# Performance work log

Measured on AMD Instinct MI355X. Metric: run time of the kernel, lower is better.

Reference implementation:

```python
import jax, jax.numpy as jnp
import numpy as np

N, D, H = 4096, 1024, 8
DH = D // H
EPS = 1e-5


def layer_norm(x, g, b):
    mu = jnp.mean(x, axis=-1, keepdims=True)
    var = jnp.mean(jnp.square(x - mu), axis=-1, keepdims=True)
    return (x - mu) * jax.lax.rsqrt(var + EPS) * g + b


def setup_inputs() -> dict:
    key = jax.random.key(0)
    ks = jax.random.split(key, 12)
    s = 0.02
    inp = {
        "x": jax.random.normal(ks[0], (N, D), dtype=jnp.float32),
        "adj": (jax.random.uniform(ks[1], (N, N)) < 0.01).astype(jnp.float32),
        "Wq": jax.random.normal(ks[2], (D, D), dtype=jnp.float32) * s,
        "Wk": jax.random.normal(ks[3], (D, D), dtype=jnp.float32) * s,
        "Wv": jax.random.normal(ks[4], (D, D), dtype=jnp.float32) * s,
        "Wo_w": jax.random.normal(ks[5], (D, D), dtype=jnp.float32) * s,
        "Wo_b": jnp.zeros((D,), dtype=jnp.float32),
        "adj_bias": jnp.full((H,), 1.0, dtype=jnp.float32),
        "ln1_g": jnp.ones((D,), dtype=jnp.float32),
        "ln1_b": jnp.zeros((D,), dtype=jnp.float32),
        "ffn_ln_g": jnp.ones((D,), dtype=jnp.float32),
        "ffn_ln_b": jnp.zeros((D,), dtype=jnp.float32),
        "ffn_w1": jax.random.normal(ks[6], (D, 2 * D), dtype=jnp.float32) * s,
        "ffn_b1": jnp.zeros((2 * D,), dtype=jnp.float32),
        "ffn_w2": jax.random.normal(ks[7], (2 * D, D), dtype=jnp.float32) * s,
        "ffn_b2": jnp.zeros((D,), dtype=jnp.float32),
    }
    return inp


def reference(x, adj, Wq, Wk, Wv, Wo_w, Wo_b, adj_bias, ln1_g, ln1_b,
              ffn_ln_g, ffn_ln_b, ffn_w1, ffn_b1, ffn_w2, ffn_b2):
    scale = DH ** -0.5
    Q = (x @ Wq).reshape(N, H, DH)
    K = (x @ Wk).reshape(N, H, DH)
    V = (x @ Wv).reshape(N, H, DH)
    # attn[i,h,j] = <Q_i, K_j> * scale + beta_h * adj[i,j]
    attn = jnp.einsum('bhd,nhd->bhn', Q, K) * scale
    attn = attn + adj_bias[None, :, None] * adj[:, None, :]
    attn = jax.nn.softmax(attn, axis=-1)  # dropout in eval mode -> identity
    out = jnp.einsum('bhn,nhd->bhd', attn, V).reshape(N, D)
    out = out @ Wo_w + Wo_b
    h = layer_norm(x + out, ln1_g, ln1_b)
    f = layer_norm(h, ffn_ln_g, ffn_ln_b)
    f = jax.nn.gelu(f @ ffn_w1 + ffn_b1, approximate=False) @ ffn_w2 + ffn_b2
    return h + f
```

## Files before the change

kernel.cpp:

```cpp
#include <hip/hip_runtime.h>
#include <hip/hip_bf16.h>
#include <cstdint>
#include <cstddef>

typedef __hip_bfloat16 bf16;
typedef __attribute__((ext_vector_type(8))) short short8;
typedef __attribute__((ext_vector_type(4))) short short4v;
typedef __attribute__((ext_vector_type(4))) float floatx4;
typedef unsigned long long u64;

#define DEVI static __device__ __forceinline__

DEVI void load_lds16(const void* g, void* l) {
  __builtin_amdgcn_global_load_lds((const __attribute__((address_space(1))) unsigned int*)g,
                                   (__attribute__((address_space(3))) unsigned int*)l, 16, 0, 0);
}
DEVI short8 ld8(const bf16* p) { return *(const short8*)p; }
DEVI floatx4 mfma16(short8 a, short8 b, floatx4 c) {
  return __builtin_amdgcn_mfma_f32_16x16x32_bf16(a, b, c, 0, 0, 0);
}
DEVI floatx4 mfma1k(short4v a, short4v b, floatx4 c) {
  return __builtin_amdgcn_mfma_f32_16x16x16bf16_1k(a, b, c, 0, 0, 0);
}
DEVI short bfb(float f) { bf16 h = __float2bfloat16(f); return __builtin_bit_cast(short, h); }
DEVI float fbf(short s) { bf16 h = __builtin_bit_cast(bf16, s); return __bfloat162float(h); }

DEVI void tr_tile(const float* in, bf16* out, int R, int C, int bx, int by) {
  __shared__ float t[32][33];
  int c0 = bx * 32, r0 = by * 32;
  int tx = threadIdx.x & 31, ty = threadIdx.x >> 5;
#pragma unroll
  for (int i = 0; i < 32; i += 8) t[ty + i][tx] = in[(size_t)(r0 + ty + i) * C + c0 + tx];
  __syncthreads();
#pragma unroll
  for (int i = 0; i < 32; i += 8)
    out[(size_t)(c0 + ty + i) * R + r0 + tx] = __float2bfloat16(t[tx][ty + i]);
}

__global__ __launch_bounds__(256)
void prep_all(const float* __restrict__ x, bf16* __restrict__ xb,
              const float* __restrict__ adj, u64* __restrict__ bits,
              const float* Wq, const float* Wk, const float* Wv, const float* Wo,
              const float* W1, const float* W2,
              bf16* Wqkvt, bf16* Wot, bf16* W1t, bf16* W2t) {
  int id = blockIdx.x;
  if (id < 4096) {
    const int row = id, tid = threadIdx.x;
    const int wave = tid >> 6, lane = tid & 63;
    float4 v = ((const float4*)(x + (size_t)row * 1024))[tid];
    bf16* o = xb + (size_t)row * 1024 + tid * 4;
    o[0] = __float2bfloat16(v.x); o[1] = __float2bfloat16(v.y);
    o[2] = __float2bfloat16(v.z); o[3] = __float2bfloat16(v.w);
    const float* arow = adj + (size_t)row * 4096;
#pragma unroll
    for (int it = 0; it < 16; it++) {
      int col = it * 256 + tid;
      u64 m = __ballot(arow[col] != 0.f);
      if (lane == 0) bits[(size_t)row * 64 + it * 4 + wave] = m;
    }
  } else if (id < 8192) {
    int q = id - 4096, w = q >> 10, t = q & 1023;
    const float* in = w == 0 ? Wq : w == 1 ? Wk : w == 2 ? Wv : Wo;
    bf16* out = w == 0 ? Wqkvt : w == 1 ? Wqkvt + 1024ull * 1024
              : w == 2 ? Wqkvt + 2048ull * 1024 : Wot;
    tr_tile(in, out, 1024, 1024, t & 31, t >> 5);
  } else if (id < 10240) {
    int t = id - 8192;
    tr_tile(W1, W1t, 1024, 2048, t & 63, t >> 6);
  } else {
    int t = id - 10240;
    tr_tile(W2, W2t, 2048, 1024, t & 31, t >> 5);
  }
}

__global__ __launch_bounds__(256)
void tr_bf16t(const bf16* __restrict__ in, bf16* __restrict__ out, int inLd) {
  __shared__ bf16 t[32][33];
  int c0 = blockIdx.x * 32, r0 = blockIdx.y * 32;
  int tx = threadIdx.x, ty = threadIdx.y;
#pragma unroll
  for (int i = 0; i < 32; i += 8) t[ty + i][tx] = in[(size_t)(r0 + ty + i) * inLd + c0 + tx];
  __syncthreads();
#pragma unroll
  for (int i = 0; i < 32; i += 8)
    out[(size_t)(c0 + ty + i) * 4096 + r0 + tx] = t[tx][ty + i];
}

template <int MODE>
__global__ __launch_bounds__(256)
void gemm_bt(const bf16* __restrict__ A, const bf16* __restrict__ Bt,
             const float* __restrict__ bias, const float* __restrict__ resid,
             float* __restrict__ outF, bf16* __restrict__ outB,
             int M, int Nn, int K) {
  __shared__ alignas(16) bf16 As[3][128 * 32];
  __shared__ alignas(16) bf16 Bs[3][128 * 32];
  const int tid = threadIdx.x;
  const int wave = tid >> 6, lane = tid & 63;
  const int m0 = blockIdx.y * 128, n0 = blockIdx.x * 128;
  const int wr = (wave >> 1) * 64, wc = (wave & 1) * 64;
  const int l15 = lane & 15, qq = lane >> 4;
  const int lr = lane >> 2, l4 = lane & 3;
  const int Kspan = K / gridDim.z;
  const int kbeg = blockIdx.z * Kspan;
  const int T = Kspan >> 5;

  floatx4 acc[4][4];
#pragma unroll
  for (int i = 0; i < 4; i++)
#pragma unroll
    for (int j = 0; j < 4; j++) acc[i][j] = (floatx4)0.f;

  const bf16* gA0 = A + (size_t)(m0 + wave * 16 + lr) * K + kbeg + l4 * 8;
  const bf16* gA1 = gA0 + (size_t)64 * K;
  const bf16* gB0 = Bt + (size_t)(n0 + wave * 16 + lr) * K + kbeg + l4 * 8;
  const bf16* gB1 = gB0 + (size_t)64 * K;
  const int lo = wave * 16 * 32;

  auto stage = [&](int t, int buf) {
    int kt = t * 32;
    load_lds16(gA0 + kt, &As[buf][lo]);
    load_lds16(gA1 + kt, &As[buf][64 * 32 + lo]);
    load_lds16(gB0 + kt, &Bs[buf][lo]);
    load_lds16(gB1 + kt, &Bs[buf][64 * 32 + lo]);
  };
  stage(0, 0);
  stage(1, 1);

  int bc = 0;
  for (int t = 0; t < T; ++t) {
    if (t < T - 1) asm volatile("s_waitcnt vmcnt(4) lgkmcnt(0)" ::: "memory");
    else           asm volatile("s_waitcnt vmcnt(0) lgkmcnt(0)" ::: "memory");
    __builtin_amdgcn_s_barrier();
    if (t + 2 < T) { int bs = bc == 0 ? 2 : bc - 1; stage(t + 2, bs); }

    short8 af[4], bfr[4];
#pragma unroll
    for (int mi = 0; mi < 4; mi++) af[mi] = ld8(&As[bc][(wr + mi * 16 + l15) * 32 + qq * 8]);
#pragma unroll
    for (int ni = 0; ni < 4; ni++) bfr[ni] = ld8(&Bs[bc][(wc + ni * 16 + l15) * 32 + qq * 8]);
#pragma unroll
    for (int mi = 0; mi < 4; mi++)
#pragma unroll
      for (int ni = 0; ni < 4; ni++)
        acc[mi][ni] = mfma16(af[mi], bfr[ni], acc[mi][ni]);
    bc = bc == 2 ? 0 : bc + 1;
  }

  const size_t zoff = (size_t)blockIdx.z * M * Nn;
#pragma unroll
  for (int mi = 0; mi < 4; mi++) {
    int row = m0 + wr + mi * 16 + qq * 4;
#pragma unroll
    for (int ni = 0; ni < 4; ni++) {
      int col = n0 + wc + ni * 16 + l15;
      float bv = 0.f;
      if (MODE == 2) bv = bias[col];
      if (MODE == 4 && blockIdx.z == 0) bv = bias[col];
#pragma unroll
      for (int r = 0; r < 4; r++) {
        float v = acc[mi][ni][r] + bv;
        size_t off = (size_t)(row + r) * Nn + col;
        if (MODE == 0) {
          outB[off] = __float2bfloat16(v);
        } else if (MODE == 2) {
          outB[off] = __float2bfloat16(0.5f * v * (1.f + erff(v * 0.70710678118654752f)));
        } else {
          if (resid && blockIdx.z == 1) v += resid[off];
          outF[zoff + off] = v;
        }
      }
    }
  }
}

__global__ __launch_bounds__(256, 2)
void attn_kernel(const bf16* __restrict__ QKV, const bf16* __restrict__ Vt,
                 const u64* __restrict__ adjbits, const float* __restrict__ adj_bias,
                 bf16* __restrict__ AOpart, float* __restrict__ lpart) {
  __shared__ alignas(16) bf16 Kf[16 * 512];
  __shared__ alignas(16) bf16 Vf[16 * 512];
  const int q0 = blockIdx.x * 128;
  const int h = blockIdx.y;
  const int split = blockIdx.z;
  const int k0 = split * 1024;
  const int tid = threadIdx.x, wave = tid >> 6, lane = tid & 63;
  const int l15 = lane & 15, qq = lane >> 4;
  const float beta = adj_bias[h];
  const float scale = 0.08838834764831845f;

  short8 qf[2][4];
#pragma unroll
  for (int mi = 0; mi < 2; mi++)
#pragma unroll
    for (int kk = 0; kk < 4; kk++)
      qf[mi][kk] = ld8(&QKV[(size_t)(q0 + wave * 32 + mi * 16 + l15) * 3072 +
                            h * 128 + kk * 32 + qq * 8]);

  floatx4 o[2][8];
#pragma unroll
  for (int mi = 0; mi < 2; mi++)
#pragma unroll
    for (int d = 0; d < 8; d++) o[mi][d] = (floatx4)0.f;
  float lrow[2] = {0.f, 0.f};

  const size_t abase = (size_t)(q0 + wave * 32 + l15) * 64 + split * 16;

  for (int t = 0; t < 16; t++) {
    const int kt = k0 + t * 64;
    __syncthreads();
#pragma unroll
    for (int i = 0; i < 4; i++) {
      int fi = wave * 4 + i;
      int ni = fi >> 2, kk = fi & 3;
      load_lds16(&QKV[(size_t)(kt + ni * 16 + l15) * 3072 + 1024 + h * 128 + kk * 32 + qq * 8],
                 (char*)Kf + fi * 1024);
      int d = fi >> 1, k2 = fi & 1;
      load_lds16(&Vt[(size_t)(h * 128 + d * 16 + l15) * 4096 + kt + k2 * 32 + qq * 8],
                 (char*)Vf + fi * 1024);
    }
    u64 ab0 = adjbits[abase + t];
    u64 ab1 = adjbits[abase + 16 * 64 + t];
    asm volatile("s_waitcnt vmcnt(0)" ::: "memory");
    __syncthreads();

#pragma unroll
    for (int ni = 0; ni < 4; ni++) {
      floatx4 s0 = (floatx4)0.f, s1 = (floatx4)0.f;
#pragma unroll
      for (int kk = 0; kk < 4; kk++) {
        short8 kf = ld8(&Kf[(ni * 4 + kk) * 512 + lane * 8]);
        s0 = mfma16(kf, qf[0][kk], s0);
        s1 = mfma16(kf, qf[1][kk], s1);
      }
      short4v pa0, pa1;
      {
        float p0, p1, p2, p3;
        int bp = ni * 16 + qq * 4;
        p0 = __expf(fmaf(s0[0], scale, ((ab0 >> (bp + 0)) & 1) ? beta : 0.f));
        p1 = __expf(fmaf(s0[1], scale, ((ab0 >> (bp + 1)) & 1) ? beta : 0.f));
        p2 = __expf(fmaf(s0[2], scale, ((ab0 >> (bp + 2)) & 1) ? beta : 0.f));
        p3 = __expf(fmaf(s0[3], scale, ((ab0 >> (bp + 3)) & 1) ? beta : 0.f));
        lrow[0] += (p0 + p1) + (p2 + p3);
        pa0.x = bfb(p0); pa0.y = bfb(p1); pa0.z = bfb(p2); pa0.w = bfb(p3);
        p0 = __expf(fmaf(s1[0], scale, ((ab1 >> (bp + 0)) & 1) ? beta : 0.f));
        p1 = __expf(fmaf(s1[1], scale, ((ab1 >> (bp + 1)) & 1) ? beta : 0.f));
        p2 = __expf(fmaf(s1[2], scale, ((ab1 >> (bp + 2)) & 1) ? beta : 0.f));
        p3 = __expf(fmaf(s1[3], scale, ((ab1 >> (bp + 3)) & 1) ? beta : 0.f));
        lrow[1] += (p0 + p1) + (p2 + p3);
        pa1.x = bfb(p0); pa1.y = bfb(p1); pa1.z = bfb(p2); pa1.w = bfb(p3);
      }
      const int voff = ((ni & 1) * 2 + (qq >> 1)) * 256 + l15 * 16 + (qq & 1) * 8;
#pragma unroll
      for (int d = 0; d < 8; d++) {
        short4v vf = *(const short4v*)((const char*)Vf + (d * 2 + (ni >> 1)) * 1024 + voff);
        o[0][d] = mfma1k(pa0, vf, o[0][d]);
        o[1][d] = mfma1k(pa1, vf, o[1][d]);
      }
    }
  }

#pragma unroll
  for (int mi = 0; mi < 2; mi++) {
    float v = lrow[mi];
    v += __shfl_xor(v, 16, 64);
    v += __shfl_xor(v, 32, 64);
    if (qq == 0) lpart[((size_t)split * 4096 + q0 + wave * 32 + mi * 16 + l15) * 8 + h] = v;
#pragma unroll
    for (int r = 0; r < 4; r++) {
      int grow = q0 + wave * 32 + mi * 16 + qq * 4 + r;
      bf16* dst = AOpart + ((size_t)split * 4096 + grow) * 1024 + h * 128;
#pragma unroll
      for (int d = 0; d < 8; d++) dst[d * 16 + l15] = __float2bfloat16(o[mi][d][r]);
    }
  }
}

__global__ __launch_bounds__(256)
void attn_norm(const bf16* __restrict__ AOpart, const float* __restrict__ lpart,
               bf16* __restrict__ AO) {
  int row = blockIdx.x, tid = threadIdx.x;
  int h = tid >> 5;
  float ls = 0.f;
#pragma unroll
  for (int s = 0; s < 4; s++) ls += lpart[((size_t)s * 4096 + row) * 8 + h];
  float a0 = 0.f, a1 = 0.f, a2 = 0.f, a3 = 0.f;
#pragma unroll
  for (int s = 0; s < 4; s++) {
    short4v v = *(const short4v*)&AOpart[((size_t)s * 4096 + row) * 1024 + tid * 4];
    a0 += fbf(v.x); a1 += fbf(v.y); a2 += fbf(v.z); a3 += fbf(v.w);
  }
  float inv = 1.f / ls;
  bf16* op = AO + (size_t)row * 1024 + tid * 4;
  op[0] = __float2bfloat16(a0 * inv);
  op[1] = __float2bfloat16(a1 * inv);
  op[2] = __float2bfloat16(a2 * inv);
  op[3] = __float2bfloat16(a3 * inv);
}

DEVI void block_sum2(float& a, float& b, float* red) {
#pragma unroll
  for (int o = 1; o < 64; o <<= 1) { a += __shfl_xor(a, o, 64); b += __shfl_xor(b, o, 64); }
  int wv = threadIdx.x >> 6;
  if ((threadIdx.x & 63) == 0) { red[wv] = a; red[4 + wv] = b; }
  __syncthreads();
  a = red[0] + red[1] + red[2] + red[3];
  b = red[4] + red[5] + red[6] + red[7];
  __syncthreads();
}

__global__ __launch_bounds__(256)
void ln2_kernel(const float* __restrict__ x, const float* __restrict__ ao0,
                const float* __restrict__ ao1,
                const float* __restrict__ g1, const float* __restrict__ b1,
                const float* __restrict__ g2, const float* __restrict__ b2,
                float* __restrict__ hout, bf16* __restrict__ fln) {
  __shared__ float red[8];
  const int row = blockIdx.x, tid = threadIdx.x;
  float4 xv = ((const float4*)(x + (size_t)row * 1024))[tid];
  float4 av = ((const float4*)(ao0 + (size_t)row * 1024))[tid];
  float4 aw = ((const float4*)(ao1 + (size_t)row * 1024))[tid];
  float s0 = xv.x + av.x + aw.x, s1 = xv.y + av.y + aw.y;
  float s2 = xv.z + av.z + aw.z, s3 = xv.w + av.w + aw.w;
  float sum = s0 + s1 + s2 + s3;
  float ssq = s0 * s0 + s1 * s1 + s2 * s2 + s3 * s3;
  block_sum2(sum, ssq, red);
  float mu = sum * (1.f / 1024.f);
  float rs = rsqrtf(ssq * (1.f / 1024.f) - mu * mu + 1e-5f);
  float4 gv = ((const float4*)g1)[tid], bv = ((const float4*)b1)[tid];
  float h0 = (s0 - mu) * rs * gv.x + bv.x;
  float h1 = (s1 - mu) * rs * gv.y + bv.y;
  float h2 = (s2 - mu) * rs * gv.z + bv.z;
  float h3 = (s3 - mu) * rs * gv.w + bv.w;
  float4 hv; hv.x = h0; hv.y = h1; hv.z = h2; hv.w = h3;
  ((float4*)(hout + (size_t)row * 1024))[tid] = hv;
  float sum2 = h0 + h1 + h2 + h3;
  float ssq2 = h0 * h0 + h1 * h1 + h2 * h2 + h3 * h3;
  block_sum2(sum2, ssq2, red);
  float mu2 = sum2 * (1.f / 1024.f);
  float rs2 = rsqrtf(ssq2 * (1.f / 1024.f) - mu2 * mu2 + 1e-5f);
  float4 g2v = ((const float4*)g2)[tid], b2v = ((const float4*)b2)[tid];
  bf16* op = fln + (size_t)row * 1024 + tid * 4;
  op[0] = __float2bfloat16((h0 - mu2) * rs2 * g2v.x + b2v.x);
  op[1] = __float2bfloat16((h1 - mu2) * rs2 * g2v.y + b2v.y);
  op[2] = __float2bfloat16((h2 - mu2) * rs2 * g2v.z + b2v.z);
  op[3] = __float2bfloat16((h3 - mu2) * rs2 * g2v.w + b2v.w);
}

__global__ __launch_bounds__(256)
void add2_kernel(const float* __restrict__ a, const float* __restrict__ b,
                 float* __restrict__ o) {
  int i = blockIdx.x * 256 + threadIdx.x;
  float4 va = ((const float4*)a)[i];
  float4 vb = ((const float4*)b)[i];
  float4 vo; vo.x = va.x + vb.x; vo.y = va.y + vb.y;
  vo.z = va.z + vb.z; vo.w = va.w + vb.w;
  ((float4*)o)[i] = vo;
}

extern "C" void kernel_launch(void* const* d_in, const int* in_sizes, int n_in,
                              void* d_out, int out_size, void* d_ws, size_t ws_size,
                              hipStream_t stream) {
  const float* x    = (const float*)d_in[0];
  const float* adj  = (const float*)d_in[1];
  const float* Wq   = (const float*)d_in[2];
  const float* Wk   = (const float*)d_in[3];
  const float* Wv   = (const float*)d_in[4];
  const float* Wo   = (const float*)d_in[5];
  const float* Wob  = (const float*)d_in[6];
  const float* adjb = (const float*)d_in[7];
  const float* g1   = (const float*)d_in[8];
  const float* b1   = (const float*)d_in[9];
  const float* g2   = (const float*)d_in[10];
  const float* b2   = (const float*)d_in[11];
  const float* W1   = (const float*)d_in[12];
  const float* fb1  = (const float*)d_in[13];
  const float* W2   = (const float*)d_in[14];
  const float* fb2  = (const float*)d_in[15];
  float* out = (float*)d_out;

  char* w = (char*)d_ws;
  size_t off = 0;
  auto take = [&](size_t bytes) {
    char* p = w + off;
    off += (bytes + 255) & ~(size_t)255;
    return p;
  };
  bf16* xb    = (bf16*)take(4096ull * 1024 * 2);
  bf16* Wqkvt = (bf16*)take(3072ull * 1024 * 2);
  bf16* Wot   = (bf16*)take(1024ull * 1024 * 2);
  bf16* W1t   = (bf16*)take(2048ull * 1024 * 2);
  bf16* W2t   = (bf16*)take(1024ull * 2048 * 2);
  bf16* QKV   = (bf16*)take(4096ull * 3072 * 2);
  bf16* Vt    = (bf16*)take(1024ull * 4096 * 2);
  bf16* AO    = (bf16*)take(4096ull * 1024 * 2);
  u64*  adjbits = (u64*)take(4096ull * 64 * 8);
  float* lpart  = (float*)take(4ull * 4096 * 8 * 4);
  char* big = take(32ull << 20);
  bf16*  AOpart = (bf16*)big;
  float* WoP    = (float*)big;
  float* F2P    = (float*)big;
  float* H   = (float*)take(4096ull * 1024 * 4);
  bf16*  FLN = (bf16*)take(4096ull * 1024 * 2);
  bf16*  G   = (bf16*)take(4096ull * 2048 * 2);

  dim3 tb(32, 8);
  prep_all<<<12288, 256, 0, stream>>>(x, xb, adj, adjbits, Wq, Wk, Wv, Wo, W1, W2,
                                      Wqkvt, Wot, W1t, W2t);
  gemm_bt<0><<<dim3(24, 32, 1), 256, 0, stream>>>(xb, Wqkvt, nullptr, nullptr,
                                                  nullptr, QKV, 4096, 3072, 1024);
  tr_bf16t<<<dim3(32, 128), tb, 0, stream>>>(QKV + 2048, Vt, 3072);
  attn_kernel<<<dim3(32, 8, 4), 256, 0, stream>>>(QKV, Vt, adjbits, adjb, AOpart, lpart);
  attn_norm<<<4096, 256, 0, stream>>>(AOpart, lpart, AO);
  gemm_bt<4><<<dim3(8, 32, 2), 256, 0, stream>>>(AO, Wot, Wob, nullptr,
                                                 WoP, nullptr, 4096, 1024, 1024);
  ln2_kernel<<<4096, 256, 0, stream>>>(x, WoP, WoP + 4096ull * 1024, g1, b1, g2, b2, H, FLN);
  gemm_bt<2><<<dim3(16, 32, 1), 256, 0, stream>>>(FLN, W1t, fb1, nullptr,
                                                  nullptr, G, 4096, 2048, 1024);
  gemm_bt<4><<<dim3(8, 32, 2), 256, 0, stream>>>(G, W2t, fb2, H,
                                                 F2P, nullptr, 4096, 1024, 2048);
  add2_kernel<<<4096, 256, 0, stream>>>(F2P, F2P + 4096ull * 1024, out);
}
```

Before: 442.3 us.

## Double-buffer K/V LDS tiles and prefetch adjacency bits in attention kernel

Each K/V tile gets two LDS buffers. The next tile's global-to-LDS loads are issued before the current tile's MFMA and softmax work, and the wait is relaxed to vmcnt(8), so load latency overlaps compute instead of stalling every iteration. The adjacency bitmask words are also prefetched one iteration ahead. The cost is double the LDS per block, which may limit occupancy, and raw s_barrier calls that rely on the hand-written waitcnt ordering being correct.

```diff
diff --git a/kernel.cpp b/kernel.cpp
--- a/kernel.cpp
+++ b/kernel.cpp
@@ -177,8 +177,8 @@
 void attn_kernel(const bf16* __restrict__ QKV, const bf16* __restrict__ Vt,
                  const u64* __restrict__ adjbits, const float* __restrict__ adj_bias,
                  bf16* __restrict__ AOpart, float* __restrict__ lpart) {
-  __shared__ alignas(16) bf16 Kf[16 * 512];
-  __shared__ alignas(16) bf16 Vf[16 * 512];
+  __shared__ alignas(16) bf16 Kf[2][16 * 512];
+  __shared__ alignas(16) bf16 Vf[2][16 * 512];
   const int q0 = blockIdx.x * 128;
   const int h = blockIdx.y;
   const int split = blockIdx.z;
@@ -205,30 +205,43 @@
 
   const size_t abase = (size_t)(q0 + wave * 32 + l15) * 64 + split * 16;
 
-  for (int t = 0; t < 16; t++) {
+  auto stage = [&](int t, int buf) {
     const int kt = k0 + t * 64;
-    __syncthreads();
 #pragma unroll
     for (int i = 0; i < 4; i++) {
       int fi = wave * 4 + i;
       int ni = fi >> 2, kk = fi & 3;
       load_lds16(&QKV[(size_t)(kt + ni * 16 + l15) * 3072 + 1024 + h * 128 + kk * 32 + qq * 8],
-                 (char*)Kf + fi * 1024);
+                 (char*)Kf[buf] + fi * 1024);
       int d = fi >> 1, k2 = fi & 1;
       load_lds16(&Vt[(size_t)(h * 128 + d * 16 + l15) * 4096 + kt + k2 * 32 + qq * 8],
-                 (char*)Vf + fi * 1024);
-    }
-    u64 ab0 = adjbits[abase + t];
-    u64 ab1 = adjbits[abase + 16 * 64 + t];
-    asm volatile("s_waitcnt vmcnt(0)" ::: "memory");
-    __syncthreads();
+                 (char*)Vf[buf] + fi * 1024);
+    }
+  };
+
+  u64 a0c = adjbits[abase + 0];
+  u64 a1c = adjbits[abase + 1024 + 0];
+  stage(0, 0);
+
+  for (int t = 0; t < 16; t++) {
+    const int buf = t & 1;
+    __builtin_amdgcn_s_barrier();
+    if (t < 15) {
+      stage(t + 1, buf ^ 1);
+      asm volatile("s_waitcnt vmcnt(8)" ::: "memory");
+    } else {
+      asm volatile("s_waitcnt vmcnt(0)" ::: "memory");
+    }
+    __builtin_amdgcn_s_barrier();
+    u64 a0n = 0, a1n = 0;
+    if (t < 15) { a0n = adjbits[abase + t + 1]; a1n = adjbits[abase + 1024 + t + 1]; }
 
 #pragma unroll
     for (int ni = 0; ni < 4; ni++) {
       floatx4 s0 = (floatx4)0.f, s1 = (floatx4)0.f;
 #pragma unroll
       for (int kk = 0; kk < 4; kk++) {
-        short8 kf = ld8(&Kf[(ni * 4 + kk) * 512 + lane * 8]);
+        short8 kf = ld8(&Kf[buf][(ni * 4 + kk) * 512 + lane * 8]);
         s0 = mfma16(kf, qf[0][kk], s0);
         s1 = mfma16(kf, qf[1][kk], s1);
       }
@@ -236,27 +249,28 @@
       {
         float p0, p1, p2, p3;
         int bp = ni * 16 + qq * 4;
-        p0 = __expf(fmaf(s0[0], scale, ((ab0 >> (bp + 0)) & 1) ? beta : 0.f));
-        p1 = __expf(fmaf(s0[1], scale, ((ab0 >> (bp + 1)) & 1) ? beta : 0.f));
-        p2 = __expf(fmaf(s0[2], scale, ((ab0 >> (bp + 2)) & 1) ? beta : 0.f));
-        p3 = __expf(fmaf(s0[3], scale, ((ab0 >> (bp + 3)) & 1) ? beta : 0.f));
+        p0 = __expf(fmaf(s0[0], scale, ((a0c >> (bp + 0)) & 1) ? beta : 0.f));
+        p1 = __expf(fmaf(s0[1], scale, ((a0c >> (bp + 1)) & 1) ? beta : 0.f));
+        p2 = __expf(fmaf(s0[2], scale, ((a0c >> (bp + 2)) & 1) ? beta : 0.f));
+        p3 = __expf(fmaf(s0[3], scale, ((a0c >> (bp + 3)) & 1) ? beta : 0.f));
         lrow[0] += (p0 + p1) + (p2 + p3);
         pa0.x = bfb(p0); pa0.y = bfb(p1); pa0.z = bfb(p2); pa0.w = bfb(p3);
-        p0 = __expf(fmaf(s1[0], scale, ((ab1 >> (bp + 0)) & 1) ? beta : 0.f));
-        p1 = __expf(fmaf(s1[1], scale, ((ab1 >> (bp + 1)) & 1) ? beta : 0.f));
-        p2 = __expf(fmaf(s1[2], scale, ((ab1 >> (bp + 2)) & 1) ? beta : 0.f));
-        p3 = __expf(fmaf(s1[3], scale, ((ab1 >> (bp + 3)) & 1) ? beta : 0.f));
+        p0 = __expf(fmaf(s1[0], scale, ((a1c >> (bp + 0)) & 1) ? beta : 0.f));
+        p1 = __expf(fmaf(s1[1], scale, ((a1c >> (bp + 1)) & 1) ? beta : 0.f));
+        p2 = __expf(fmaf(s1[2], scale, ((a1c >> (bp + 2)) & 1) ? beta : 0.f));
+        p3 = __expf(fmaf(s1[3], scale, ((a1c >> (bp + 3)) & 1) ? beta : 0.f));
         lrow[1] += (p0 + p1) + (p2 + p3);
         pa1.x = bfb(p0); pa1.y = bfb(p1); pa1.z = bfb(p2); pa1.w = bfb(p3);
       }
       const int voff = ((ni & 1) * 2 + (qq >> 1)) * 256 + l15 * 16 + (qq & 1) * 8;
 #pragma unroll
       for (int d = 0; d < 8; d++) {
-        short4v vf = *(const short4v*)((const char*)Vf + (d * 2 + (ni >> 1)) * 1024 + voff);
+        short4v vf = *(const short4v*)((const char*)Vf[buf] + (d * 2 + (ni >> 1)) * 1024 + voff);
         o[0][d] = mfma1k(pa0, vf, o[0][d]);
         o[1][d] = mfma1k(pa1, vf, o[1][d]);
       }
     }
+    a0c = a0n; a1c = a1n;
   }
 
 #pragma unroll
```

Result: no change. 445.7 us (+0.8%).

## Replace split-K GEMMs with 128x64 tiles and fuse residual into epilogue

Applied to the files above, without the earlier changes.

The Wo and FFN2 GEMMs drop split-K over two z-slices, which wrote fp32 partials. They now use a 128x64 output tile so the grid stays at 512 blocks. The FFN2 epilogue adds the residual H and writes the final output directly, which removes the add2 kernel. ln2 reads one attention-output buffer instead of two, cutting fp32 partial traffic and one launch at the cost of smaller N tiles with less B reuse.

```diff
diff --git a/kernel.cpp b/kernel.cpp
--- a/kernel.cpp
+++ b/kernel.cpp
@@ -86,33 +86,32 @@
     out[(size_t)(c0 + ty + i) * 4096 + r0 + tx] = t[tx][ty + i];
 }
 
-template <int MODE>
+template <int MODE, int BN>
 __global__ __launch_bounds__(256)
 void gemm_bt(const bf16* __restrict__ A, const bf16* __restrict__ Bt,
              const float* __restrict__ bias, const float* __restrict__ resid,
              float* __restrict__ outF, bf16* __restrict__ outB,
              int M, int Nn, int K) {
+  constexpr int NI = BN / 32;
   __shared__ alignas(16) bf16 As[3][128 * 32];
-  __shared__ alignas(16) bf16 Bs[3][128 * 32];
+  __shared__ alignas(16) bf16 Bs[3][BN * 32];
   const int tid = threadIdx.x;
   const int wave = tid >> 6, lane = tid & 63;
-  const int m0 = blockIdx.y * 128, n0 = blockIdx.x * 128;
-  const int wr = (wave >> 1) * 64, wc = (wave & 1) * 64;
+  const int m0 = blockIdx.y * 128, n0 = blockIdx.x * BN;
+  const int wr = (wave >> 1) * 64, wc = (wave & 1) * (BN / 2);
   const int l15 = lane & 15, qq = lane >> 4;
   const int lr = lane >> 2, l4 = lane & 3;
-  const int Kspan = K / gridDim.z;
-  const int kbeg = blockIdx.z * Kspan;
-  const int T = Kspan >> 5;
-
-  floatx4 acc[4][4];
+  const int T = K >> 5;
+
+  floatx4 acc[4][NI];
 #pragma unroll
   for (int i = 0; i < 4; i++)
 #pragma unroll
-    for (int j = 0; j < 4; j++) acc[i][j] = (floatx4)0.f;
-
-  const bf16* gA0 = A + (size_t)(m0 + wave * 16 + lr) * K + kbeg + l4 * 8;
+    for (int j = 0; j < NI; j++) acc[i][j] = (floatx4)0.f;
+
+  const bf16* gA0 = A + (size_t)(m0 + wave * 16 + lr) * K + l4 * 8;
   const bf16* gA1 = gA0 + (size_t)64 * K;
-  const bf16* gB0 = Bt + (size_t)(n0 + wave * 16 + lr) * K + kbeg + l4 * 8;
+  const bf16* gB0 = Bt + (size_t)(n0 + wave * 16 + lr) * K + l4 * 8;
   const bf16* gB1 = gB0 + (size_t)64 * K;
   const int lo = wave * 16 * 32;
 
@@ -121,41 +120,44 @@
     load_lds16(gA0 + kt, &As[buf][lo]);
     load_lds16(gA1 + kt, &As[buf][64 * 32 + lo]);
     load_lds16(gB0 + kt, &Bs[buf][lo]);
-    load_lds16(gB1 + kt, &Bs[buf][64 * 32 + lo]);
+    if (BN == 128) load_lds16(gB1 + kt, &Bs[buf][64 * 32 + lo]);
   };
   stage(0, 0);
   stage(1, 1);
 
   int bc = 0;
   for (int t = 0; t < T; ++t) {
-    if (t < T - 1) asm volatile("s_waitcnt vmcnt(4) lgkmcnt(0)" ::: "memory");
-    else           asm volatile("s_waitcnt vmcnt(0) lgkmcnt(0)" ::: "memory");
+    if (t < T - 1) {
+      if constexpr (BN == 128)
+        asm volatile("s_waitcnt vmcnt(4) lgkmcnt(0)" ::: "memory");
+      else
+        asm volatile("s_waitcnt vmcnt(3) lgkmcnt(0)" ::: "memory");
+    } else {
+      asm volatile("s_waitcnt vmcnt(0) lgkmcnt(0)" ::: "memory");
+    }
     __builtin_amdgcn_s_barrier();
     if (t + 2 < T) { int bs = bc == 0 ? 2 : bc - 1; stage(t + 2, bs); }
 
-    short8 af[4], bfr[4];
+    short8 af[4], bfr[NI];
 #pragma unroll
     for (int mi = 0; mi < 4; mi++) af[mi] = ld8(&As[bc][(wr + mi * 16 + l15) * 32 + qq * 8]);
 #pragma unroll
-    for (int ni = 0; ni < 4; ni++) bfr[ni] = ld8(&Bs[bc][(wc + ni * 16 + l15) * 32 + qq * 8]);
+    for (int ni = 0; ni < NI; ni++) bfr[ni] = ld8(&Bs[bc][(wc + ni * 16 + l15) * 32 + qq * 8]);
 #pragma unroll
     for (int mi = 0; mi < 4; mi++)
 #pragma unroll
-      for (int ni = 0; ni < 4; ni++)
+      for (int ni = 0; ni < NI; ni++)
         acc[mi][ni] = mfma16(af[mi], bfr[ni], acc[mi][ni]);
     bc = bc == 2 ? 0 : bc + 1;
   }
 
-  const size_t zoff = (size_t)blockIdx.z * M * Nn;
 #pragma unroll
   for (int mi = 0; mi < 4; mi++) {
     int row = m0 + wr + mi * 16 + qq * 4;
 #pragma unroll
-    for (int ni = 0; ni < 4; ni++) {
+    for (int ni = 0; ni < NI; ni++) {
       int col = n0 + wc + ni * 16 + l15;
-      float bv = 0.f;
-      if (MODE == 2) bv = bias[col];
-      if (MODE == 4 && blockIdx.z == 0) bv = bias[col];
+      float bv = (MODE >= 1) ? bias[col] : 0.f;
 #pragma unroll
       for (int r = 0; r < 4; r++) {
         float v = acc[mi][ni][r] + bv;
@@ -164,9 +166,10 @@
           outB[off] = __float2bfloat16(v);
         } else if (MODE == 2) {
           outB[off] = __float2bfloat16(0.5f * v * (1.f + erff(v * 0.70710678118654752f)));
+        } else if (MODE == 1) {
+          outF[off] = v;
         } else {
-          if (resid && blockIdx.z == 1) v += resid[off];
-          outF[zoff + off] = v;
+          outF[off] = v + resid[off];
         }
       }
     }
@@ -219,7 +222,7 @@
                  (char*)Vf + fi * 1024);
     }
     u64 ab0 = adjbits[abase + t];
-    u64 ab1 = adjbits[abase + 16 * 64 + t];
+    u64 ab1 = adjbits[abase + 1024 + t];
     asm volatile("s_waitcnt vmcnt(0)" ::: "memory");
     __syncthreads();
 
@@ -309,18 +312,15 @@
 }
 
 __global__ __launch_bounds__(256)
-void ln2_kernel(const float* __restrict__ x, const float* __restrict__ ao0,
-                const float* __restrict__ ao1,
+void ln2_kernel(const float* __restrict__ x, const float* __restrict__ ao,
                 const float* __restrict__ g1, const float* __restrict__ b1,
                 const float* __restrict__ g2, const float* __restrict__ b2,
                 float* __restrict__ hout, bf16* __restrict__ fln) {
   __shared__ float red[8];
   const int row = blockIdx.x, tid = threadIdx.x;
   float4 xv = ((const float4*)(x + (size_t)row * 1024))[tid];
-  float4 av = ((const float4*)(ao0 + (size_t)row * 1024))[tid];
-  float4 aw = ((const float4*)(ao1 + (size_t)row * 1024))[tid];
-  float s0 = xv.x + av.x + aw.x, s1 = xv.y + av.y + aw.y;
-  float s2 = xv.z + av.z + aw.z, s3 = xv.w + av.w + aw.w;
+  float4 av = ((const float4*)(ao + (size_t)row * 1024))[tid];
+  float s0 = xv.x + av.x, s1 = xv.y + av.y, s2 = xv.z + av.z, s3 = xv.w + av.w;
   float sum = s0 + s1 + s2 + s3;
   float ssq = s0 * s0 + s1 * s1 + s2 * s2 + s3 * s3;
   block_sum2(sum, ssq, red);
@@ -346,17 +346,6 @@
   op[3] = __float2bfloat16((h3 - mu2) * rs2 * g2v.w + b2v.w);
 }
 
-__global__ __launch_bounds__(256)
-void add2_kernel(const float* __restrict__ a, const float* __restrict__ b,
-                 float* __restrict__ o) {
-  int i = blockIdx.x * 256 + threadIdx.x;
-  float4 va = ((const float4*)a)[i];
-  float4 vb = ((const float4*)b)[i];
-  float4 vo; vo.x = va.x + vb.x; vo.y = va.y + vb.y;
-  vo.z = va.z + vb.z; vo.w = va.w + vb.w;
-  ((float4*)o)[i] = vo;
-}
-
 extern "C" void kernel_launch(void* const* d_in, const int* in_sizes, int n_in,
                               void* d_out, int out_size, void* d_ws, size_t ws_size,
                               hipStream_t stream) {
@@ -398,7 +387,6 @@
   char* big = take(32ull << 20);
   bf16*  AOpart = (bf16*)big;
   float* WoP    = (float*)big;
-  float* F2P    = (float*)big;
   float* H   = (float*)take(4096ull * 1024 * 4);
   bf16*  FLN = (bf16*)take(4096ull * 1024 * 2);
   bf16*  G   = (bf16*)take(4096ull * 2048 * 2);
@@ -406,17 +394,16 @@
   dim3 tb(32, 8);
   prep_all<<<12288, 256, 0, stream>>>(x, xb, adj, adjbits, Wq, Wk, Wv, Wo, W1, W2,
                                       Wqkvt, Wot, W1t, W2t);
-  gemm_bt<0><<<dim3(24, 32, 1), 256, 0, stream>>>(xb, Wqkvt, nullptr, nullptr,
-                                                  nullptr, QKV, 4096, 3072, 1024);
+  gemm_bt<0, 128><<<dim3(24, 32), 256, 0, stream>>>(xb, Wqkvt, nullptr, nullptr,
+                                                    nullptr, QKV, 4096, 3072, 1024);
   tr_bf16t<<<dim3(32, 128), tb, 0, stream>>>(QKV + 2048, Vt, 3072);
   attn_kernel<<<dim3(32, 8, 4), 256, 0, stream>>>(QKV, Vt, adjbits, adjb, AOpart, lpart);
   attn_norm<<<4096, 256, 0, stream>>>(AOpart, lpart, AO);
-  gemm_bt<4><<<dim3(8, 32, 2), 256, 0, stream>>>(AO, Wot, Wob, nullptr,
-                                                 WoP, nullptr, 4096, 1024, 1024);
-  ln2_kernel<<<4096, 256, 0, stream>>>(x, WoP, WoP + 4096ull * 1024, g1, b1, g2, b2, H, FLN);
-  gemm_bt<2><<<dim3(16, 32, 1), 256, 0, stream>>>(FLN, W1t, fb1, nullptr,
-                                                  nullptr, G, 4096, 2048, 1024);
-  gemm_bt<4><<<dim3(8, 32, 2), 256, 0, stream>>>(G, W2t, fb2, H,
-                                                 F2P, nullptr, 4096, 1024, 2048);
-  add2_kernel<<<4096, 256, 0, stream>>>(F2P, F2P + 4096ull * 1024, out);
-}
+  gemm_bt<1, 64><<<dim3(16, 32), 256, 0, stream>>>(AO, Wot, Wob, nullptr,
+                                                   WoP, nullptr, 4096, 1024, 1024);
+  ln2_kernel<<<4096, 256, 0, stream>>>(x, WoP, g1, b1, g2, b2, H, FLN);
+  gemm_bt<2, 128><<<dim3(16, 32), 256, 0, stream>>>(FLN, W1t, fb1, nullptr,
+                                                    nullptr, G, 4096, 2048, 1024);
+  gemm_bt<3, 64><<<dim3(16, 32), 256, 0, stream>>>(G, W2t, fb2, H,
+                                                   out, nullptr, 4096, 1024, 2048);
+}
```

New measurement: 434.2 us. About the same (-1.8%).
